# Performance work log

Measured on AMD Instinct MI355X. Metric: run time of the kernel, lower is better.

Reference implementation:

```python
import jax, jax.numpy as jnp
import numpy as np

INT_MIN = jnp.iinfo(jnp.int32).min


def setup_inputs() -> dict:
    key = jax.random.key(0)
    ks = jax.random.split(key, 12)
    N, E, H, R, T = 200000, 100000, 100, 172, 100
    return {
        'src': jax.random.randint(ks[0], (E,), 0, N, dtype=jnp.int32),
        'dst': jax.random.randint(ks[1], (E,), 0, N, dtype=jnp.int32),
        't': jax.random.randint(ks[2], (E,), 0, 1000000, dtype=jnp.int32),
        'raw_msg': jax.random.normal(ks[3], (E, R), dtype=jnp.float32),
        'memory': jax.random.normal(ks[4], (N, H), dtype=jnp.float32),
        'last_update': jax.random.randint(ks[5], (N,), 0, 1000, dtype=jnp.int32),
        'te_w': jax.random.normal(ks[6], (T, 1), dtype=jnp.float32) * 0.1,
        'te_b': jax.random.normal(ks[7], (T,), dtype=jnp.float32) * 0.1,
        'w_ih': jax.random.normal(ks[8], (3 * H, 2 * H + R + T), dtype=jnp.float32) * 0.05,
        'w_hh': jax.random.normal(ks[9], (3 * H, H), dtype=jnp.float32) * 0.05,
        'b_ih': jax.random.normal(ks[10], (3 * H,), dtype=jnp.float32) * 0.05,
        'b_hh': jax.random.normal(ks[11], (3 * H,), dtype=jnp.float32) * 0.05,
    }


def reference(src, dst, t, raw_msg, memory, last_update, te_w, te_b, w_ih, w_hh, b_ih, b_hh):
    N, H = memory.shape
    E = src.shape[0]

    def time_enc(t_rel):  # Linear(1, time_dim) then cos, t_rel: [E] float
        return jnp.cos(t_rel[:, None] * te_w[:, 0][None, :] + te_b[None, :])

    # IdentityMessage: concat(mem[src], mem[dst], raw_msg, t_enc); two streams (s and d)
    t_enc_s = time_enc((t - last_update[src]).astype(raw_msg.dtype))
    t_enc_d = time_enc((t - last_update[dst]).astype(raw_msg.dtype))
    msg_s = jnp.concatenate([memory[src], memory[dst], raw_msg, t_enc_s], axis=-1)
    msg_d = jnp.concatenate([memory[dst], memory[src], raw_msg, t_enc_d], axis=-1)

    msg = jnp.concatenate([msg_s, msg_d], axis=0)        # [2E, msg_dim]
    idx = jnp.concatenate([src, dst], axis=0)            # [2E]
    t2 = jnp.concatenate([t, t], axis=0)                 # [2E]

    # LastAggregator: per node pick the message with maximum timestamp
    max_t = jnp.full((N,), INT_MIN, dtype=t2.dtype).at[idx].max(t2)
    cand = jnp.where(t2 == max_t[idx], jnp.arange(2 * E, dtype=jnp.int32), jnp.int32(-1))
    win = jnp.full((N,), -1, dtype=jnp.int32).at[idx].max(cand)  # winning edge per node
    has_msg = win >= 0
    aggr = jnp.where(has_msg[:, None], msg[jnp.clip(win, 0)], 0.0)  # [N, msg_dim]

    # GRUCell(msg_dim, H)
    gi = aggr @ w_ih.T + b_ih                             # [N, 3H]
    gh = memory @ w_hh.T + b_hh                           # [N, 3H]
    i_r, i_z, i_n = jnp.split(gi, 3, axis=-1)
    h_r, h_z, h_n = jnp.split(gh, 3, axis=-1)
    r = jax.nn.sigmoid(i_r + h_r)
    z = jax.nn.sigmoid(i_z + h_z)
    n = jnp.tanh(i_n + r * h_n)
    memory_new = (1.0 - z) * n + z * memory               # [N, H]

    last_update_new = last_update.at[idx].max(t2)         # scatter latest event time
    return memory_new, last_update_new
```

## Files before the change

kernel.cpp:

```cpp
#include <hip/hip_runtime.h>
#include <math.h>

typedef __attribute__((ext_vector_type(8))) short  short8;
typedef __attribute__((ext_vector_type(4))) float  f32x4;

static constexpr int H     = 100;
static constexpr int RD    = 172;
static constexpr int WK    = 472;
static constexpr int MSTR  = 104;
static constexpr int RSTR  = 176;
static constexpr int NKS   = 20;
static constexpr int MB    = 32;
static constexpr int GRPS  = 2;
static constexpr int BLK   = 448;
static constexpr int NTT   = 28;
static constexpr int BPK_N = NTT * NKS * 64 * 8;

static constexpr int FB_MB = 48;
static constexpr int FB_GR = 3;

__device__ inline unsigned short f2bf(float x) {
    union { float f; unsigned u; } v; v.f = x;
    return (unsigned short)((v.u + 0x7FFFu + ((v.u >> 16) & 1u)) >> 16);
}
__device__ inline float bf2f(unsigned short b) {
    union { unsigned u; float f; } v; v.u = ((unsigned)b) << 16;
    return v.f;
}
__device__ inline unsigned pkbf(float a, float b) {
    unsigned r;
    asm("v_cvt_pk_bf16_f32 %0, %1, %2" : "=v"(r) : "v"(a), "v"(b));
    return r;
}
__device__ inline float frcp(float x) {
    float r;
    asm("v_rcp_f32 %0, %1" : "=v"(r) : "v"(x));
    return r;
}
__device__ inline f32x4 mfma16(short8 a, short8 b, f32x4 c) {
    return __builtin_amdgcn_mfma_f32_16x16x32_bf16(a, b, c, 0, 0, 0);
}
__device__ inline float4 ld4g(const float* base, int lc, int limit) {
    if (lc + 4 <= limit) return *(const float4*)(base + lc);
    return make_float4(0.f, 0.f, 0.f, 0.f);
}
__device__ inline void gl16(const unsigned short* g, unsigned short* l) {
    __builtin_amdgcn_global_load_lds(
        (const __attribute__((address_space(1))) void*)g,
        (__attribute__((address_space(3))) void*)l, 16, 0, 0);
}

__global__ __launch_bounds__(256) void k_pre(
    const float* __restrict__ mem, const float* __restrict__ raw,
    const float* __restrict__ w_ih, const float* __restrict__ w_hh,
    unsigned short* __restrict__ memB, unsigned short* __restrict__ rawB,
    unsigned short* __restrict__ B, int* __restrict__ maxt, int* __restrict__ win,
    int* __restrict__ zb, int N, int E, int docvt)
{
    int i = blockIdx.x * 256 + threadIdx.x;
    if (docvt) {
        const int nm = N * 13;
        if (i < nm) {
            int row = i / 13, o = (i - row * 13) * 8;
            float4 a = ld4g(mem + (size_t)row * 100, o, 100);
            float4 b = ld4g(mem + (size_t)row * 100, o + 4, 100);
            int4 s; s.x = (int)pkbf(a.x, a.y); s.y = (int)pkbf(a.z, a.w);
            s.z = (int)pkbf(b.x, b.y); s.w = (int)pkbf(b.z, b.w);
            *(int4*)&memB[(size_t)row * MSTR + o] = s;
            return;
        }
        i -= nm;
        const int nr = E * 22;
        if (i < nr) {
            int row = i / 22, o = (i - row * 22) * 8;
            float4 a = ld4g(raw + (size_t)row * 172, o, 172);
            float4 b = ld4g(raw + (size_t)row * 172, o + 4, 172);
            int4 s; s.x = (int)pkbf(a.x, a.y); s.y = (int)pkbf(a.z, a.w);
            s.z = (int)pkbf(b.x, b.y); s.w = (int)pkbf(b.z, b.w);
            *(int4*)&rawB[(size_t)row * RSTR + o] = s;
            return;
        }
        i -= nr;
    }
    if (i < BPK_N) {
        int idx  = i;
        int jj   = idx & 7;
        int lane = (idx >> 3) & 63;
        int rest = idx >> 9;
        int ks   = rest % NKS;
        int tile = rest / NKS;
        int kk   = ks * 32 + ((lane >> 4) << 3) + jj;
        float v = 0.f;
        if (tile < 21) {
            int gate = tile / 7;
            int tcol = (tile % 7) * 16 + (lane & 15);
            if (tcol < 100) {
                if (kk < 512) {
                    int col = -1;
                    if (kk < 100)                   col = kk;
                    else if (kk >= 104 && kk < 204) col = kk - 4;
                    else if (kk >= 208 && kk < 380) col = kk - 8;
                    else if (kk >= 384 && kk < 484) col = kk - 12;
                    if (col >= 0) v = w_ih[(gate * 100 + tcol) * WK + col];
                } else {
                    int khh = kk - 512;
                    if (gate < 2 && khh < 100)
                        v = w_hh[(gate * 100 + tcol) * H + khh];
                }
            }
        } else {
            int tcol = (tile - 21) * 16 + (lane & 15);
            int khh  = kk - 512;
            if (tcol < 100 && khh >= 0 && khh < 100)
                v = w_hh[(200 + tcol) * H + khh];
        }
        B[idx] = f2bf(v);
        return;
    }
    i -= BPK_N;
    if (i < N) { maxt[i] = (int)0x80000000; win[i] = -1; }
    if (i < 128) zb[i] = 0;
}

__global__ __launch_bounds__(256) void k_maxt(const int* __restrict__ src, const int* __restrict__ dst,
                                              const int* __restrict__ t, int* __restrict__ maxt, int E) {
    int j = blockIdx.x * blockDim.x + threadIdx.x;
    if (j < E) {
        int tj = t[j];
        atomicMax(&maxt[src[j]], tj);
        atomicMax(&maxt[dst[j]], tj);
    }
}
__global__ __launch_bounds__(256) void k_win(const int* __restrict__ src, const int* __restrict__ dst,
                                             const int* __restrict__ t, const int* __restrict__ maxt,
                                             int* __restrict__ win, int E) {
    int j = blockIdx.x * blockDim.x + threadIdx.x;
    if (j < E) {
        int tj = t[j];
        int s = src[j], d = dst[j];
        if (maxt[s] == tj) atomicMax(&win[s], j);
        if (maxt[d] == tj) atomicMax(&win[d], j + E);
    }
}
__global__ __launch_bounds__(256) void k_meta(const int* __restrict__ src, const int* __restrict__ dst,
                                              const int* __restrict__ t, const int* __restrict__ last_update,
                                              const int* __restrict__ win, int4* __restrict__ meta,
                                              float* __restrict__ out_lu, int E, int N) {
    int i = blockIdx.x * blockDim.x + threadIdx.x;
    if (i >= N) return;
    int lu = last_update[i], w = win[i];
    int j = 0, other = 0, has = 0, te = lu; float dt = 0.f;
    if (w >= 0) {
        has = 1;
        int e = (w < E) ? w : (w - E);
        j = e;
        other = (w < E) ? dst[e] : src[e];
        te = t[e];
        dt = (float)(te - lu);
    }
    out_lu[i] = (float)(te > lu ? te : lu);
    int4 m; m.x = j; m.y = other; m.z = has; m.w = __float_as_int(dt);
    meta[i] = m;
}

#define LB(tile, ks) (*(const short8*)&Bpack[(((size_t)(tile) * NKS + (ks)) * 64 + lane) * 8])

__global__ __launch_bounds__(BLK, 4) void k_gru2(
    const unsigned short* __restrict__ memB, const unsigned short* __restrict__ rawB,
    const float* __restrict__ te_w, const float* __restrict__ te_b,
    const float* __restrict__ b_ih, const float* __restrict__ b_hh,
    const int4* __restrict__ meta, const unsigned short* __restrict__ zb,
    const unsigned short* __restrict__ Bpack,
    float* __restrict__ out_mem, int N)
{
    __shared__ unsigned short sA[GRPS * NKS * 512];

    const int tid  = threadIdx.x;
    const int wv   = tid >> 6;
    const int lane = tid & 63;
    const int q    = lane >> 4;
    const int row  = lane & 15;
    const int node0 = blockIdx.x * MB;

#pragma unroll
    for (int g = 0; g < GRPS; ++g) {
        const int node_g = node0 + g * 16 + row;
        const bool val = node_g < N;
        const int4 m = val ? meta[node_g] : make_int4(0, 0, 0, 0);
        const bool has = m.z != 0;
        const float dt = __int_as_float(m.w);
        const unsigned short* pmm = has ? memB + (size_t)node_g * MSTR : zb;
        const unsigned short* pot = has ? memB + (size_t)m.y * MSTR   : zb;
        const unsigned short* prw = has ? rawB + (size_t)m.x * RSTR   : zb;
        const unsigned short* phh = val ? memB + (size_t)node_g * MSTR : zb;

#pragma unroll
        for (int ii = 0; ii < 3; ++ii) {
            const int ks = wv + 7 * ii;
            if (ks < NKS && (ks < 12 || ks >= 16)) {
                const int k0 = ks * 32 + q * 8;
                const unsigned short* s =
                    (k0 < 104) ? pmm + k0 :
                    (k0 < 208) ? pot + (k0 - 104) :
                    (k0 < 384) ? prw + (k0 - 208) :
                                 phh + (k0 - 512);
                gl16(s, &sA[(g * NKS + ks) * 512]);
            }
        }
#pragma unroll
        for (int ii = 0; ii < 3; ++ii) {
            const int ks = wv + 7 * ii;
            if (ks >= 12 && ks < 16) {
                const int o = (ks - 12) * 32 + q * 8;
                float4 w0 = ld4g(te_w, o, 100), w1 = ld4g(te_w, o + 4, 100);
                float4 c0 = ld4g(te_b, o, 100), c1 = ld4g(te_b, o + 4, 100);
                const float hf = has ? 1.f : 0.f;
                float v0 = hf * __cosf(fmaf(dt, w0.x, c0.x));
                float v1 = hf * __cosf(fmaf(dt, w0.y, c0.y));
                float v2 = hf * __cosf(fmaf(dt, w0.z, c0.z));
                float v3 = hf * __cosf(fmaf(dt, w0.w, c0.w));
                float v4 = hf * __cosf(fmaf(dt, w1.x, c1.x));
                float v5 = hf * __cosf(fmaf(dt, w1.y, c1.y));
                float v6 = hf * __cosf(fmaf(dt, w1.z, c1.z));
                float v7 = hf * __cosf(fmaf(dt, w1.w, c1.w));
                int4 sv;
                sv.x = (int)pkbf(v0, v1); sv.y = (int)pkbf(v2, v3);
                sv.z = (int)pkbf(v4, v5); sv.w = (int)pkbf(v6, v7);
                *(int4*)&sA[(g * NKS + ks) * 512 + lane * 8] = sv;
            }
        }
    }
    __syncthreads();

    f32x4 ar[GRPS], az[GRPS], an[GRPS], ah[GRPS];
#pragma unroll
    for (int m = 0; m < GRPS; ++m) { ar[m] = (f32x4)0.f; az[m] = (f32x4)0.f; an[m] = (f32x4)0.f; ah[m] = (f32x4)0.f; }

    short8 cr = LB(wv, 0);
    short8 cz = LB(7 + wv, 0);
    short8 cn = LB(14 + wv, 0);

    __builtin_amdgcn_s_setprio(1);
#pragma unroll
    for (int ks = 0; ks < NKS; ++ks) {
        short8 nr = cr, nz = cz, nn2 = cn;
        if (ks + 1 < NKS) {
            nr  = LB(wv, ks + 1);
            nz  = LB(7 + wv, ks + 1);
            nn2 = LB((ks + 1 < 16) ? (14 + wv) : (21 + wv), ks + 1);
        }
        short8 a0 = *(const short8*)&sA[(0 * NKS + ks) * 512 + lane * 8];
        short8 a1 = *(const short8*)&sA[(1 * NKS + ks) * 512 + lane * 8];
        __builtin_amdgcn_sched_barrier(0);
        ar[0] = mfma16(a0, cr, ar[0]);  ar[1] = mfma16(a1, cr, ar[1]);
        az[0] = mfma16(a0, cz, az[0]);  az[1] = mfma16(a1, cz, az[1]);
        if (ks < 16) { an[0] = mfma16(a0, cn, an[0]);  an[1] = mfma16(a1, cn, an[1]); }
        else         { ah[0] = mfma16(a0, cn, ah[0]);  ah[1] = mfma16(a1, cn, ah[1]); }
        cr = nr; cz = nz; cn = nn2;
    }
    __builtin_amdgcn_s_setprio(0);

    const int c = wv * 16 + row;
    if (c < 100) {
        const float br_ = b_ih[c]       + b_hh[c];
        const float bz_ = b_ih[c + 100] + b_hh[c + 100];
        const float bin = b_ih[c + 200];
        const float bhn = b_hh[c + 200];
        const int ksh = 16 + (c >> 5);
        const int qh  = (c >> 3) & 3;
        const int e   = c & 7;
#pragma unroll
        for (int m = 0; m < GRPS; ++m) {
#pragma unroll
            for (int r = 0; r < 4; ++r) {
                const int node = node0 + m * 16 + q * 4 + r;
                if (node < N) {
                    const int rw = q * 4 + r;
                    const float h  = bf2f(sA[(m * NKS + ksh) * 512 + (qh * 16 + rw) * 8 + e]);
                    const float rg = frcp(1.f + __expf(-(ar[m][r] + br_)));
                    const float zg = frcp(1.f + __expf(-(az[m][r] + bz_)));
                    const float xn = an[m][r] + bin + rg * (ah[m][r] + bhn);
                    const float th = copysignf(1.f - 2.f * frcp(__expf(2.f * fabsf(xn)) + 1.f), xn);
                    out_mem[(size_t)node * H + c] = (1.f - zg) * th + zg * h;
                }
            }
        }
    }
}

__global__ __launch_bounds__(BLK, 4) void k_gru_fused(
    const int* __restrict__ src, const int* __restrict__ dst, const int* __restrict__ t,
    const float* __restrict__ raw_msg, const float* __restrict__ memory,
    const int* __restrict__ last_update, const float* __restrict__ te_w,
    const float* __restrict__ te_b, const float* __restrict__ b_ih,
    const float* __restrict__ b_hh, const int* __restrict__ win,
    const unsigned short* __restrict__ Bpack,
    float* __restrict__ out_mem, float* __restrict__ out_lu, int E, int N)
{
    __shared__ unsigned short sA[FB_GR * NKS * 512];
    __shared__ int   s_other[FB_MB];
    __shared__ int   s_j[FB_MB];
    __shared__ int   s_has[FB_MB];
    __shared__ float s_dt[FB_MB];

    const int tid   = threadIdx.x;
    const int node0 = blockIdx.x * FB_MB;

    if (tid < FB_MB) {
        int node = node0 + tid;
        int has = 0, j = 0, other = 0; float dt = 0.f;
        if (node < N) {
            int lu = last_update[node];
            int w  = win[node];
            int te = lu;
            if (w >= 0) {
                has = 1;
                int e = (w < E) ? w : (w - E);
                j = e;
                other = (w < E) ? dst[e] : src[e];
                te = t[e];
                dt = (float)(te - lu);
            }
            out_lu[node] = (float)(te > lu ? te : lu);
        }
        s_j[tid] = j; s_other[tid] = other; s_has[tid] = has; s_dt[tid] = dt;
    }
    __syncthreads();

    if (tid < 432) {
        const int nl    = tid % 48;
        const int c0    = tid / 48;
        const int node  = node0 + nl;
        const bool valid = node < N;
        const int has   = s_has[nl];
        const float* memN = memory + (size_t)node * H;
        const float* memO = memory + (size_t)s_other[nl] * H;
        const float* rawJ = raw_msg + (size_t)s_j[nl] * RD;
        const float dt  = s_dt[nl];
        const int grp = nl >> 4;
        const int row = nl & 15;

        float4 va[8], vb[8];
#pragma unroll
        for (int it = 0; it < 8; ++it) {
            const int cc = c0 + it * 9;
            va[it] = make_float4(0.f, 0.f, 0.f, 0.f); vb[it] = va[it];
            if (cc < 67) {
                const int c = cc + 13, kb = c * 8;
                if (c < 26)      { if (has)  { va[it] = ld4g(memO, kb - 104, 100); vb[it] = ld4g(memO, kb - 100, 100); } }
                else if (c < 48) { if (has)  { va[it] = ld4g(rawJ, kb - 208, RD ); vb[it] = ld4g(rawJ, kb - 204, RD ); } }
                else if (c < 64) { }
                else             { if (valid){ va[it] = ld4g(memN, kb - 512, 100); vb[it] = ld4g(memN, kb - 508, 100); } }
            }
        }
#pragma unroll
        for (int it = 0; it < 8; ++it) {
            const int cc = c0 + it * 9;
            if (cc < 67) {
                const int c = cc + 13;
                if (c >= 48 && c < 64 && has) {
                    const int lc = c * 8 - 384;
                    float vv[8];
#pragma unroll
                    for (int x = 0; x < 8; ++x) {
                        int col = lc + x;
                        vv[x] = (col < 100) ? __cosf(fmaf(dt, te_w[col], te_b[col])) : 0.f;
                    }
                    va[it] = make_float4(vv[0], vv[1], vv[2], vv[3]);
                    vb[it] = make_float4(vv[4], vv[5], vv[6], vv[7]);
                }
                int4 sv;
                sv.x = (int)pkbf(va[it].x, va[it].y);
                sv.y = (int)pkbf(va[it].z, va[it].w);
                sv.z = (int)pkbf(vb[it].x, vb[it].y);
                sv.w = (int)pkbf(vb[it].z, vb[it].w);
                {
                    const int ks = c >> 2, sub = c & 3;
                    *(int4*)&sA[((grp * NKS + ks) * 64 + sub * 16 + row) * 8] = sv;
                }
                if (c >= 64 && c < 77) {
                    int4 sm_;
                    sm_.x = has ? sv.x : 0; sm_.y = has ? sv.y : 0;
                    sm_.z = has ? sv.z : 0; sm_.w = has ? sv.w : 0;
                    const int cm = c - 64;
                    const int ks = cm >> 2, sub = cm & 3;
                    *(int4*)&sA[((grp * NKS + ks) * 64 + sub * 16 + row) * 8] = sm_;
                }
            }
        }
    }
    __syncthreads();

    const int wv   = tid >> 6;
    const int lane = tid & 63;
    const int lrow = lane & 15;
    const int lhi  = lane >> 4;

    f32x4 ar[FB_GR], az[FB_GR], an[FB_GR], ah[FB_GR];
#pragma unroll
    for (int m = 0; m < FB_GR; ++m) { ar[m] = (f32x4)0.f; az[m] = (f32x4)0.f; an[m] = (f32x4)0.f; ah[m] = (f32x4)0.f; }

    __builtin_amdgcn_s_setprio(1);
#pragma unroll
    for (int ks = 0; ks < NKS; ++ks) {
        short8 a0 = *(const short8*)&sA[(0 * NKS + ks) * 512 + lane * 8];
        short8 a1 = *(const short8*)&sA[(1 * NKS + ks) * 512 + lane * 8];
        short8 a2 = *(const short8*)&sA[(2 * NKS + ks) * 512 + lane * 8];
        short8 br = LB(wv, ks);
        short8 bz = LB(7 + wv, ks);
        short8 bn = (ks < 16) ? LB(14 + wv, ks) : LB(21 + wv, ks);
        ar[0] = mfma16(a0, br, ar[0]);  ar[1] = mfma16(a1, br, ar[1]);  ar[2] = mfma16(a2, br, ar[2]);
        az[0] = mfma16(a0, bz, az[0]);  az[1] = mfma16(a1, bz, az[1]);  az[2] = mfma16(a2, bz, az[2]);
        if (ks < 16) { an[0] = mfma16(a0, bn, an[0]);  an[1] = mfma16(a1, bn, an[1]);  an[2] = mfma16(a2, bn, an[2]); }
        else         { ah[0] = mfma16(a0, bn, ah[0]);  ah[1] = mfma16(a1, bn, ah[1]);  ah[2] = mfma16(a2, bn, ah[2]); }
    }
    __builtin_amdgcn_s_setprio(0);

    const int c = wv * 16 + lrow;
    if (c < 100) {
        const float br_ = b_ih[c]       + b_hh[c];
        const float bz_ = b_ih[c + 100] + b_hh[c + 100];
        const float bin = b_ih[c + 200];
        const float bhn = b_hh[c + 200];
        const int ksh = 16 + (c >> 5);
        const int qh  = (c >> 3) & 3;
        const int e   = c & 7;
#pragma unroll
        for (int m = 0; m < FB_GR; ++m) {
#pragma unroll
            for (int r = 0; r < 4; ++r) {
                const int node = node0 + m * 16 + lhi * 4 + r;
                if (node < N) {
                    const int rw = lhi * 4 + r;
                    const float h  = bf2f(sA[(m * NKS + ksh) * 512 + (qh * 16 + rw) * 8 + e]);
                    const float rg = frcp(1.f + __expf(-(ar[m][r] + br_)));
                    const float zg = frcp(1.f + __expf(-(az[m][r] + bz_)));
                    const float xn = an[m][r] + bin + rg * (ah[m][r] + bhn);
                    const float th = copysignf(1.f - 2.f * frcp(__expf(2.f * fabsf(xn)) + 1.f), xn);
                    out_mem[(size_t)node * H + c] = (1.f - zg) * th + zg * h;
                }
            }
        }
    }
}

extern "C" void kernel_launch(void* const* d_in, const int* in_sizes, int n_in,
                              void* d_out, int out_size, void* d_ws, size_t ws_size,
                              hipStream_t stream)
{
    const int*   src         = (const int*)d_in[0];
    const int*   dst         = (const int*)d_in[1];
    const int*   t           = (const int*)d_in[2];
    const float* raw_msg     = (const float*)d_in[3];
    const float* memory      = (const float*)d_in[4];
    const int*   last_update = (const int*)d_in[5];
    const float* te_w        = (const float*)d_in[6];
    const float* te_b        = (const float*)d_in[7];
    const float* w_ih        = (const float*)d_in[8];
    const float* w_hh        = (const float*)d_in[9];
    const float* b_ih        = (const float*)d_in[10];
    const float* b_hh        = (const float*)d_in[11];

    const int E = in_sizes[0];
    const int N = in_sizes[5];

    float* out    = (float*)d_out;
    float* out_lu = out + (size_t)N * H;

    char* ws = (char*)d_ws;
    int* maxt = (int*)ws;
    int* win  = maxt + N;
    unsigned short* Bpack = (unsigned short*)(win + N);
    int4* meta = (int4*)(Bpack + BPK_N);
    unsigned short* zb   = (unsigned short*)(meta + N);
    unsigned short* memB = zb + 256;
    unsigned short* rawB = memB + (size_t)N * MSTR + 32;
    const size_t need = (size_t)((char*)(rawB + (size_t)E * RSTR) - ws) + 64;

    if (ws_size >= need) {
        const int npre = N * 13 + E * 22 + BPK_N + N;
        k_pre <<<(npre + 255) / 256, 256, 0, stream>>>(memory, raw_msg, w_ih, w_hh,
                                                       memB, rawB, Bpack, maxt, win, (int*)zb, N, E, 1);
        k_maxt<<<(E + 255) / 256, 256, 0, stream>>>(src, dst, t, maxt, E);
        k_win <<<(E + 255) / 256, 256, 0, stream>>>(src, dst, t, maxt, win, E);
        k_meta<<<(N + 255) / 256, 256, 0, stream>>>(src, dst, t, last_update, win, meta, out_lu, E, N);
        k_gru2<<<(N + MB - 1) / MB, BLK, 0, stream>>>(memB, rawB, te_w, te_b, b_ih, b_hh,
                                                      meta, zb, Bpack, out, N);
    } else {
        const int npre = BPK_N + N;
        k_pre <<<(npre + 255) / 256, 256, 0, stream>>>(memory, raw_msg, w_ih, w_hh,
                                                       Bpack, Bpack, Bpack, maxt, win, (int*)zb, N, E, 0);
        k_maxt<<<(E + 255) / 256, 256, 0, stream>>>(src, dst, t, maxt, E);
        k_win <<<(E + 255) / 256, 256, 0, stream>>>(src, dst, t, maxt, win, E);
        k_gru_fused<<<(N + FB_MB - 1) / FB_MB, BLK, 0, stream>>>(src, dst, t, raw_msg, memory, last_update,
                                                                 te_w, te_b, b_ih, b_hh, win, Bpack,
                                                                 out, out_lu, E, N);
    }
}
```

Before: 196.6 us.

## Make GRU kernel persistent over several tiles with double-buffered LDS staging

```diff
diff --git a/kernel.cpp b/kernel.cpp
--- a/kernel.cpp
+++ b/kernel.cpp
@@ -13,6 +13,8 @@
 static constexpr int MB    = 32;
 static constexpr int GRPS  = 2;
 static constexpr int BLK   = 448;
+static constexpr int TPB   = 4;
+static constexpr int ABUF  = GRPS * NKS * 512;
 static constexpr int NTT   = 28;
 static constexpr int BPK_N = NTT * NKS * 64 * 8;
 
@@ -165,23 +167,13 @@
 
 #define LB(tile, ks) (*(const short8*)&Bpack[(((size_t)(tile) * NKS + (ks)) * 64 + lane) * 8])
 
-__global__ __launch_bounds__(BLK, 4) void k_gru2(
-    const unsigned short* __restrict__ memB, const unsigned short* __restrict__ rawB,
+__device__ inline void stage_tile(
+    int node0, unsigned short* __restrict__ buf,
+    const int4* __restrict__ meta, const unsigned short* __restrict__ memB,
+    const unsigned short* __restrict__ rawB, const unsigned short* __restrict__ zb,
     const float* __restrict__ te_w, const float* __restrict__ te_b,
-    const float* __restrict__ b_ih, const float* __restrict__ b_hh,
-    const int4* __restrict__ meta, const unsigned short* __restrict__ zb,
-    const unsigned short* __restrict__ Bpack,
-    float* __restrict__ out_mem, int N)
+    int N, int wv, int lane, int q, int row)
 {
-    __shared__ unsigned short sA[GRPS * NKS * 512];
-
-    const int tid  = threadIdx.x;
-    const int wv   = tid >> 6;
-    const int lane = tid & 63;
-    const int q    = lane >> 4;
-    const int row  = lane & 15;
-    const int node0 = blockIdx.x * MB;
-
 #pragma unroll
     for (int g = 0; g < GRPS; ++g) {
         const int node_g = node0 + g * 16 + row;
@@ -204,7 +196,7 @@
                     (k0 < 208) ? pot + (k0 - 104) :
                     (k0 < 384) ? prw + (k0 - 208) :
                                  phh + (k0 - 512);
-                gl16(s, &sA[(g * NKS + ks) * 512]);
+                gl16(s, &buf[(g * NKS + ks) * 512]);
             }
         }
 #pragma unroll
@@ -226,65 +218,94 @@
                 int4 sv;
                 sv.x = (int)pkbf(v0, v1); sv.y = (int)pkbf(v2, v3);
                 sv.z = (int)pkbf(v4, v5); sv.w = (int)pkbf(v6, v7);
-                *(int4*)&sA[(g * NKS + ks) * 512 + lane * 8] = sv;
-            }
-        }
-    }
+                *(int4*)&buf[(g * NKS + ks) * 512 + lane * 8] = sv;
+            }
+        }
+    }
+}
+
+__global__ __launch_bounds__(BLK, 4) void k_gru3(
+    const unsigned short* __restrict__ memB, const unsigned short* __restrict__ rawB,
+    const float* __restrict__ te_w, const float* __restrict__ te_b,
+    const float* __restrict__ b_ih, const float* __restrict__ b_hh,
+    const int4* __restrict__ meta, const unsigned short* __restrict__ zb,
+    const unsigned short* __restrict__ Bpack,
+    float* __restrict__ out_mem, int N)
+{
+    __shared__ unsigned short sA[2 * ABUF];
+
+    const int tid  = threadIdx.x;
+    const int wv   = tid >> 6;
+    const int lane = tid & 63;
+    const int q    = lane >> 4;
+    const int row  = lane & 15;
+
+    const int ntiles    = (N + MB - 1) / MB;
+    const int tile_base = blockIdx.x * TPB;
+    const int ntl       = min(TPB, ntiles - tile_base);
+    if (ntl <= 0) return;
+
+    const int c   = wv * 16 + row;
+    const bool cv = c < 100;
+    const float br_ = cv ? b_ih[c]       + b_hh[c]       : 0.f;
+    const float bz_ = cv ? b_ih[c + 100] + b_hh[c + 100] : 0.f;
+    const float bin = cv ? b_ih[c + 200] : 0.f;
+    const float bhn = cv ? b_hh[c + 200] : 0.f;
+    const int ksh = 16 + (c >> 5);
+    const int qh  = (c >> 3) & 3;
+    const int e   = c & 7;
+
+    stage_tile(tile_base * MB, sA, meta, memB, rawB, zb, te_w, te_b, N, wv, lane, q, row);
     __syncthreads();
 
-    f32x4 ar[GRPS], az[GRPS], an[GRPS], ah[GRPS];
-#pragma unroll
-    for (int m = 0; m < GRPS; ++m) { ar[m] = (f32x4)0.f; az[m] = (f32x4)0.f; an[m] = (f32x4)0.f; ah[m] = (f32x4)0.f; }
-
-    short8 cr = LB(wv, 0);
-    short8 cz = LB(7 + wv, 0);
-    short8 cn = LB(14 + wv, 0);
-
-    __builtin_amdgcn_s_setprio(1);
-#pragma unroll
-    for (int ks = 0; ks < NKS; ++ks) {
-        short8 nr = cr, nz = cz, nn2 = cn;
-        if (ks + 1 < NKS) {
-            nr  = LB(wv, ks + 1);
-            nz  = LB(7 + wv, ks + 1);
-            nn2 = LB((ks + 1 < 16) ? (14 + wv) : (21 + wv), ks + 1);
-        }
-        short8 a0 = *(const short8*)&sA[(0 * NKS + ks) * 512 + lane * 8];
-        short8 a1 = *(const short8*)&sA[(1 * NKS + ks) * 512 + lane * 8];
+    for (int i = 0; i < ntl; ++i) {
+        unsigned short* bufc = sA + (i & 1) * ABUF;
+        unsigned short* bufn = sA + ((i + 1) & 1) * ABUF;
+        const int node0 = (tile_base + i) * MB;
+
+        if (i + 1 < ntl)
+            stage_tile(node0 + MB, bufn, meta, memB, rawB, zb, te_w, te_b, N, wv, lane, q, row);
         __builtin_amdgcn_sched_barrier(0);
-        ar[0] = mfma16(a0, cr, ar[0]);  ar[1] = mfma16(a1, cr, ar[1]);
-        az[0] = mfma16(a0, cz, az[0]);  az[1] = mfma16(a1, cz, az[1]);
-        if (ks < 16) { an[0] = mfma16(a0, cn, an[0]);  an[1] = mfma16(a1, cn, an[1]); }
-        else         { ah[0] = mfma16(a0, cn, ah[0]);  ah[1] = mfma16(a1, cn, ah[1]); }
-        cr = nr; cz = nz; cn = nn2;
-    }
-    __builtin_amdgcn_s_setprio(0);
-
-    const int c = wv * 16 + row;
-    if (c < 100) {
-        const float br_ = b_ih[c]       + b_hh[c];
-        const float bz_ = b_ih[c + 100] + b_hh[c + 100];
-        const float bin = b_ih[c + 200];
-        const float bhn = b_hh[c + 200];
-        const int ksh = 16 + (c >> 5);
-        const int qh  = (c >> 3) & 3;
-        const int e   = c & 7;
-#pragma unroll
-        for (int m = 0; m < GRPS; ++m) {
-#pragma unroll
-            for (int r = 0; r < 4; ++r) {
-                const int node = node0 + m * 16 + q * 4 + r;
-                if (node < N) {
-                    const int rw = q * 4 + r;
-                    const float h  = bf2f(sA[(m * NKS + ksh) * 512 + (qh * 16 + rw) * 8 + e]);
-                    const float rg = frcp(1.f + __expf(-(ar[m][r] + br_)));
-                    const float zg = frcp(1.f + __expf(-(az[m][r] + bz_)));
-                    const float xn = an[m][r] + bin + rg * (ah[m][r] + bhn);
-                    const float th = copysignf(1.f - 2.f * frcp(__expf(2.f * fabsf(xn)) + 1.f), xn);
-                    out_mem[(size_t)node * H + c] = (1.f - zg) * th + zg * h;
+
+        f32x4 ar[GRPS], az[GRPS], an[GRPS], ah[GRPS];
+#pragma unroll
+        for (int m = 0; m < GRPS; ++m) { ar[m] = (f32x4)0.f; az[m] = (f32x4)0.f; an[m] = (f32x4)0.f; ah[m] = (f32x4)0.f; }
+
+        __builtin_amdgcn_s_setprio(1);
+#pragma unroll
+        for (int ks = 0; ks < NKS; ++ks) {
+            short8 a0 = *(const short8*)&bufc[(0 * NKS + ks) * 512 + lane * 8];
+            short8 a1 = *(const short8*)&bufc[(1 * NKS + ks) * 512 + lane * 8];
+            short8 br = LB(wv, ks);
+            short8 bz = LB(7 + wv, ks);
+            short8 bn = (ks < 16) ? LB(14 + wv, ks) : LB(21 + wv, ks);
+            ar[0] = mfma16(a0, br, ar[0]);  ar[1] = mfma16(a1, br, ar[1]);
+            az[0] = mfma16(a0, bz, az[0]);  az[1] = mfma16(a1, bz, az[1]);
+            if (ks < 16) { an[0] = mfma16(a0, bn, an[0]);  an[1] = mfma16(a1, bn, an[1]); }
+            else         { ah[0] = mfma16(a0, bn, ah[0]);  ah[1] = mfma16(a1, bn, ah[1]); }
+        }
+        __builtin_amdgcn_s_setprio(0);
+
+        if (cv) {
+#pragma unroll
+            for (int m = 0; m < GRPS; ++m) {
+#pragma unroll
+                for (int r = 0; r < 4; ++r) {
+                    const int node = node0 + m * 16 + q * 4 + r;
+                    if (node < N) {
+                        const int rw = q * 4 + r;
+                        const float h  = bf2f(bufc[(m * NKS + ksh) * 512 + (qh * 16 + rw) * 8 + e]);
+                        const float rg = frcp(1.f + __expf(-(ar[m][r] + br_)));
+                        const float zg = frcp(1.f + __expf(-(az[m][r] + bz_)));
+                        const float xn = an[m][r] + bin + rg * (ah[m][r] + bhn);
+                        const float th = copysignf(1.f - 2.f * frcp(__expf(2.f * fabsf(xn)) + 1.f), xn);
+                        out_mem[(size_t)node * H + c] = (1.f - zg) * th + zg * h;
+                    }
                 }
             }
         }
+
+        __syncthreads();
     }
 }
 
@@ -484,8 +505,10 @@
         k_maxt<<<(E + 255) / 256, 256, 0, stream>>>(src, dst, t, maxt, E);
         k_win <<<(E + 255) / 256, 256, 0, stream>>>(src, dst, t, maxt, win, E);
         k_meta<<<(N + 255) / 256, 256, 0, stream>>>(src, dst, t, last_update, win, meta, out_lu, E, N);
-        k_gru2<<<(N + MB - 1) / MB, BLK, 0, stream>>>(memB, rawB, te_w, te_b, b_ih, b_hh,
-                                                      meta, zb, Bpack, out, N);
+        const int ntiles = (N + MB - 1) / MB;
+        const int nblk   = (ntiles + TPB - 1) / TPB;
+        k_gru3<<<nblk, BLK, 0, stream>>>(memB, rawB, te_w, te_b, b_ih, b_hh,
+                                         meta, zb, Bpack, out, N);
     } else {
         const int npre = BPK_N + N;
         k_pre <<<(npre + 255) / 256, 256, 0, stream>>>(memory, raw_msg, w_ih, w_hh,
```

Measured after the change: 506.8 us. +157.8%, slower.
